# Optimization experiments

Measured on AMD Instinct MI355X. Metric: run time of the kernel, lower is better.

## Reference

```python
import jax, jax.numpy as jnp
import numpy as np

IN_DIM = 32000   # source vocab
OUT_DIM = 32000  # target vocab
HID = 1024
MAXLEN = 32      # decode steps
B = 64
SRC_LEN = 256


def _lstm_bias(h):
    # Keras LSTM: unit_forget_bias=True -> forget-gate bias = 1, rest 0. Gate order i,f,g,o.
    return jnp.concatenate([jnp.zeros(h), jnp.ones(h), jnp.zeros(2 * h)])


def setup_inputs() -> dict:
    key = jax.random.key(0)
    ks = jax.random.split(key, 12)
    g = lambda k, shape, s=0.02: (jax.random.normal(k, shape, jnp.float32) * s)
    return {
        "source": jax.random.randint(ks[0], (B, SRC_LEN), 0, IN_DIM, jnp.int32),
        "enc_emb": g(ks[1], (IN_DIM, HID)),
        "enc_K": g(ks[2], (HID, 4 * HID)),
        "enc_R": g(ks[3], (HID, 4 * HID)),
        "enc_b": _lstm_bias(HID),
        "dec_emb": g(ks[4], (OUT_DIM, HID)),
        "dec_K": g(ks[5], (HID, 4 * HID)),
        "dec_R": g(ks[6], (HID, 4 * HID)),
        "dec_b": _lstm_bias(HID),
        "W_a": g(ks[7], (HID, HID)),
        "W_c": g(ks[8], (2 * HID, HID)),
        "b_c": jnp.zeros(HID, jnp.float32),
        "W_out": g(ks[9], (HID, OUT_DIM)),
        "b_out": jnp.zeros(OUT_DIM, jnp.float32),
    }


def _lstm_cell(x, h, c, K, R, b):
    z = x @ K + h @ R + b
    i, f, g, o = jnp.split(z, 4, axis=-1)
    c = jax.nn.sigmoid(f) * c + jax.nn.sigmoid(i) * jnp.tanh(g)
    h = jax.nn.sigmoid(o) * jnp.tanh(c)
    return h, c


def reference(source, enc_emb, enc_K, enc_R, enc_b,
              dec_emb, dec_K, dec_R, dec_b,
              W_a, W_c, b_c, W_out, b_out):
    bsz = source.shape[0]
    hid = enc_K.shape[0]

    # ----- Encoder (mask_zero=True: skip state update where source==0) -----
    xe = enc_emb[source]                      # [B,T,H]
    mask = source > 0                         # [B,T]

    def enc_step(carry, xm):
        h, c = carry
        x, m = xm                             # x [B,H], m [B]
        hn, cn = _lstm_cell(x, h, c, enc_K, enc_R, enc_b)
        m = m[:, None]
        return (jnp.where(m, hn, h), jnp.where(m, cn, c)), jnp.where(m, hn, h)

    h0 = jnp.zeros((bsz, hid), xe.dtype)
    (he, ce), hs_t = jax.lax.scan(enc_step, (h0, h0),
                                  (xe.transpose(1, 0, 2), mask.T))
    hs = hs_t.transpose(1, 0, 2)              # [B,T,H] encoder states

    # ----- Decoder loop (greedy argmax feedback) -----
    hsW = hs @ W_a                            # [B,T,H], precomputed attention keys
    amask = mask[:, None, :].astype(hs.dtype)  # [B,1,T]

    def dec_step(carry, _):
        y, h, c = carry                       # y [B] int32
        x = dec_emb[y]                        # [B,H]
        hn, cn = _lstm_cell(x, h, c, dec_K, dec_R, dec_b)
        ht = hn[:, None, :]                   # [B,1,H]
        # Luong attention with source mask (exp -> mask -> normalize, as in source)
        sc = jnp.einsum('bqh,bkh->bqk', ht, hsW)        # [B,1,T]
        sc = jnp.exp(sc - sc.max(-1, keepdims=True)) * amask
        a = sc / sc.sum(-1, keepdims=True)
        ctx = jnp.einsum('bqk,bkh->bqh', a, hs)          # [B,1,H]
        ah = jnp.tanh(jnp.concatenate([ctx, ht], -1) @ W_c + b_c)
        prob = jax.nn.softmax(ah @ W_out + b_out, axis=-1)[:, 0, :]  # [B,V]
        yn = jnp.argmax(prob, axis=-1).astype(jnp.int32)
        return (yn, hn, cn), prob

    y0 = jnp.ones((bsz,), jnp.int32)          # start token = 1 (tf.ones)
    _, outs = jax.lax.scan(dec_step, (y0, he, ce), None, length=MAXLEN)
    return outs.transpose(1, 0, 2)            # [B, MAXLEN, OUT_DIM]
```

## Files before the change

kernel.cpp:

```cpp
#include <hip/hip_runtime.h>
#include <hip/hip_bf16.h>

typedef __hip_bfloat16 bf16;
typedef short bf8v __attribute__((ext_vector_type(8)));
typedef float f32x4 __attribute__((ext_vector_type(4)));

#define DEVINL __device__ __forceinline__
#define MFMA16(a, b, c) __builtin_amdgcn_mfma_f32_16x16x32_bf16((a), (b), (c), 0, 0, 0)

DEVINL float us2f(unsigned short u) { unsigned v = ((unsigned)u) << 16; return __uint_as_float(v); }
DEVINL float b2f(bf16 x) { return __bfloat162float(x); }
DEVINL bf16 f2b(float x) { return __float2bfloat16(x); }
DEVINL float sigf(float x) { return 1.0f / (1.0f + expf(-x)); }
DEVINL unsigned short f2bu(float f) { bf16 h = __float2bfloat16(f); return *(unsigned short*)&h; }

DEVINL void gload16(const void* g, void* l) {
  __builtin_amdgcn_global_load_lds((const __attribute__((address_space(1))) void*)g,
                                   (__attribute__((address_space(3))) void*)l, 16, 0, 0);
}

DEVINL unsigned ald(const unsigned* p) {
  return __hip_atomic_load(p, __ATOMIC_RELAXED, __HIP_MEMORY_SCOPE_AGENT);
}
DEVINL void ast(unsigned* p, unsigned v) {
  __hip_atomic_store(p, v, __ATOMIC_RELAXED, __HIP_MEMORY_SCOPE_AGENT);
}
DEVINL float aldf(const float* p) { unsigned u = ald((const unsigned*)p); return __uint_as_float(u); }
DEVINL void astf(float* p, float v) { ast((unsigned*)p, __float_as_uint(v)); }

DEVINL void gridbar2(unsigned* bars, unsigned lgen) {
  __syncthreads();
  if (threadIdx.x == 0) {
    unsigned s = lgen & 1;
    unsigned g = blockIdx.x >> 5;
    unsigned* grp = bars + (g * 2 + s) * 16;
    unsigned* top = bars + (16 + s) * 16;
    unsigned* gen = bars + 288;
    unsigned t = __hip_atomic_fetch_add(grp, 1u, __ATOMIC_RELAXED, __HIP_MEMORY_SCOPE_AGENT);
    if (t == 31u) {
      ast(grp, 0u);
      unsigned tt = __hip_atomic_fetch_add(top, 1u, __ATOMIC_RELAXED, __HIP_MEMORY_SCOPE_AGENT);
      if (tt == 7u) {
        ast(top, 0u);
        asm volatile("s_waitcnt vmcnt(0)");
        ast(gen, lgen + 1u);
      }
    }
    while (ald(gen) <= lgen) __builtin_amdgcn_s_sleep(4);
  }
  __syncthreads();
}

DEVINL void bar64(unsigned* b, unsigned lgen, int lid) {
  __syncthreads();
  if (threadIdx.x == 0) {
    unsigned s = lgen & 1;
    unsigned* grp = b + (((unsigned)(lid >> 5) & 1u) * 2 + s) * 16;
    unsigned* top = b + (4 + s) * 16;
    unsigned* gen = b + 96;
    unsigned t = __hip_atomic_fetch_add(grp, 1u, __ATOMIC_RELAXED, __HIP_MEMORY_SCOPE_AGENT);
    if (t == 31u) {
      ast(grp, 0u);
      unsigned tt = __hip_atomic_fetch_add(top, 1u, __ATOMIC_RELAXED, __HIP_MEMORY_SCOPE_AGENT);
      if (tt == 1u) {
        ast(top, 0u);
        asm volatile("s_waitcnt vmcnt(0)");
        ast(gen, lgen + 1u);
      }
    }
    while (ald(gen) <= lgen) __builtin_amdgcn_s_sleep(2);
  }
  __syncthreads();
}

#define OKPT_H  ((size_t)0)
#define OKPT_L  ((size_t)8388608)
#define ORPT_H  ((size_t)16777216)
#define ORPT_L  ((size_t)25165824)
#define OWAT    ((size_t)33554432)
#define OXE_H   ((size_t)35651584)
#define OXE_L   ((size_t)69206016)
#define OHSF5   ((size_t)35651584)
#define OHSB5   ((size_t)102760448)
#define XCH     ((size_t)136314880)
#define OHPK_E0 (XCH + 0)
#define OHPK_E1 (XCH + 262144)
#define OHPK_D0 (XCH + 524288)
#define OCBUF5  (XCH + 1048576)
#define OAHPK   (XCH + 1310720)
#define ORSUM5  (XCH + 1572864)
#define ORMAX5  (XCH + 1638400)
#define ORIDX5  (XCH + 1769472)
#define OPSUM5  (XCH + 1900544)
#define OBARS5  (XCH + 1901568)
#define OXK_L5  ((size_t)138412032)
#define OWCT_H  ((size_t)0)
#define OWCT_L  ((size_t)4194304)
#define OPCTX5  ((size_t)8388608)
#define OWOT5   ((size_t)138412032)
#define OKRTH5  ((size_t)203948032)
#define OKRTL5  ((size_t)220725248)
#define OHSW5   ((size_t)237502464)

#define DELTA   1e-4f

#define D_LH   0
#define D_LL   32768
#define D_ZS   65536
#define D_KBH  83968
#define D_KBL  116736
#define D4_A   0
#define D4_W   16384
#define D4_E   49152
#define D_HBF  0
#define D_PSC  4096
#define D_EK   8448
#define D_PC4  8704
#define D_ZS3  0
#define D_PSC2 0
#define D_GMX  4352
#define D_CCN  8512
#define D_CAND 8576
#define D_YL   149504
#define D_INV  149568
#define D_RT   149632

__global__ void ed_zero_v6(float4* p, int n) {
  int i = blockIdx.x * 256 + threadIdx.x;
  if (i < n) p[i] = make_float4(0.f, 0.f, 0.f, 0.f);
}

__global__ void ed_transpose_v6(const float* __restrict__ in, bf16* __restrict__ out,
                                int R, int C, int ostride, int ooff, int perm) {
  __shared__ float tile[32][33];
  int c0 = blockIdx.x * 32, r0 = blockIdx.y * 32;
  int tx = threadIdx.x & 31, ty0 = threadIdx.x >> 5;
#pragma unroll
  for (int i = 0; i < 4; i++) {
    int ty = ty0 + i * 8;
    tile[ty][tx] = in[(size_t)(r0 + ty) * C + c0 + tx];
  }
  __syncthreads();
#pragma unroll
  for (int i = 0; i < 4; i++) {
    int ty = ty0 + i * 8;
    int c = c0 + ty;
    int oc = perm ? ((c & 1023) * 4 + (c >> 10)) : c;
    out[(size_t)oc * ostride + ooff + r0 + tx] = f2b(tile[tx][ty]);
  }
}

__global__ void ed_transpose_split_v6(const float* __restrict__ in, bf16* __restrict__ oh,
                                      bf16* __restrict__ ol, int R, int C, int ostride,
                                      int ooff, int perm) {
  __shared__ float tile[32][33];
  int c0 = blockIdx.x * 32, r0 = blockIdx.y * 32;
  int tx = threadIdx.x & 31, ty0 = threadIdx.x >> 5;
#pragma unroll
  for (int i = 0; i < 4; i++) {
    int ty = ty0 + i * 8;
    tile[ty][tx] = in[(size_t)(r0 + ty) * C + c0 + tx];
  }
  __syncthreads();
#pragma unroll
  for (int i = 0; i < 4; i++) {
    int ty = ty0 + i * 8;
    int c = c0 + ty;
    int oc = perm ? ((c & 1023) * 4 + (c >> 10)) : c;
    float v = tile[tx][ty];
    bf16 hh = f2b(v);
    size_t o = (size_t)oc * ostride + ooff + r0 + tx;
    oh[o] = hh;
    ol[o] = f2b(v - b2f(hh));
  }
}

__global__ void ed_gather_split_v6(const int* __restrict__ src, const float* __restrict__ emb,
                                   bf16* __restrict__ xh, bf16* __restrict__ xl) {
  int bid = blockIdx.x;
  int t = bid >> 6, b = bid & 63;
  int tok = src[b * 256 + t];
  const float* rowp = emb + (size_t)tok * 1024;
  int i = threadIdx.x * 4;
  float4 v = *(const float4*)(rowp + i);
  bf16 h0 = f2b(v.x), h1 = f2b(v.y), h2 = f2b(v.z), h3 = f2b(v.w);
  ushort4 oh, ol;
  oh.x = *(unsigned short*)&h0; oh.y = *(unsigned short*)&h1;
  oh.z = *(unsigned short*)&h2; oh.w = *(unsigned short*)&h3;
  ol.x = f2bu(v.x - b2f(h0)); ol.y = f2bu(v.y - b2f(h1));
  ol.z = f2bu(v.z - b2f(h2)); ol.w = f2bu(v.w - b2f(h3));
  *(ushort4*)(xh + (size_t)bid * 1024 + i) = oh;
  *(ushort4*)(xl + (size_t)bid * 1024 + i) = ol;
}

__global__ __launch_bounds__(256, 2) void ed_gemm_bt_v6(
    const bf16* __restrict__ A, const bf16* __restrict__ BT, bf16* __restrict__ C,
    int M, int N, int K) {
  __shared__ __align__(16) bf16 As[128 * 32];
  __shared__ __align__(16) bf16 Bs[128 * 32];
  int m0 = blockIdx.y * 128, n0 = blockIdx.x * 128;
  int tid = threadIdx.x, w = tid >> 6, l = tid & 63;
  int wm = w >> 1, wn = w & 1;
  int lr = l & 15, lq = l >> 4;
  f32x4 acc[4][4] = {};
  for (int k0 = 0; k0 < K; k0 += 32) {
    __syncthreads();
#pragma unroll
    for (int j = 0; j < 2; j++) {
      int o = (w * 2 + j) * 1024 + l * 16;
      int rrow = o >> 6, kk = (o & 63) >> 1;
      gload16(A + (size_t)(m0 + rrow) * K + k0 + kk, (char*)As + (w * 2 + j) * 1024);
      gload16(BT + (size_t)(n0 + rrow) * K + k0 + kk, (char*)Bs + (w * 2 + j) * 1024);
    }
    __syncthreads();
#pragma unroll
    for (int mi = 0; mi < 4; mi++) {
      bf8v a = *(const bf8v*)(As + (wm * 64 + mi * 16 + lr) * 32 + lq * 8);
#pragma unroll
      for (int ni = 0; ni < 4; ni++) {
        bf8v b = *(const bf8v*)(Bs + (wn * 64 + ni * 16 + lr) * 32 + lq * 8);
        acc[mi][ni] = MFMA16(a, b, acc[mi][ni]);
      }
    }
  }
#pragma unroll
  for (int mi = 0; mi < 4; mi++)
#pragma unroll
    for (int ni = 0; ni < 4; ni++)
#pragma unroll
      for (int r = 0; r < 4; r++)
        C[(size_t)(m0 + wm * 64 + mi * 16 + lq * 4 + r) * N + n0 + wn * 64 + ni * 16 + lr] =
            f2b(acc[mi][ni][r]);
}

__global__ __launch_bounds__(256, 2) void ed_gemm3_v6(
    const bf16* __restrict__ Ah, const bf16* __restrict__ Al,
    const bf16* __restrict__ Bh, const bf16* __restrict__ Bl,
    bf16* __restrict__ Ch, bf16* __restrict__ Cl, int M, int N, int K) {
  __shared__ __align__(16) bf16 Ash[128 * 32];
  __shared__ __align__(16) bf16 Asl[128 * 32];
  __shared__ __align__(16) bf16 Bsh[128 * 32];
  __shared__ __align__(16) bf16 Bsl[128 * 32];
  int m0 = blockIdx.y * 128, n0 = blockIdx.x * 128;
  int tid = threadIdx.x, w = tid >> 6, l = tid & 63;
  int wm = w >> 1, wn = w & 1;
  int lr = l & 15, lq = l >> 4;
  f32x4 acc[4][4] = {};
  for (int k0 = 0; k0 < K; k0 += 32) {
    __syncthreads();
#pragma unroll
    for (int j = 0; j < 2; j++) {
      int o = (w * 2 + j) * 1024 + l * 16;
      int rrow = o >> 6, kk = (o & 63) >> 1;
      gload16(Ah + (size_t)(m0 + rrow) * K + k0 + kk, (char*)Ash + (w * 2 + j) * 1024);
      gload16(Al + (size_t)(m0 + rrow) * K + k0 + kk, (char*)Asl + (w * 2 + j) * 1024);
      gload16(Bh + (size_t)(n0 + rrow) * K + k0 + kk, (char*)Bsh + (w * 2 + j) * 1024);
      gload16(Bl + (size_t)(n0 + rrow) * K + k0 + kk, (char*)Bsl + (w * 2 + j) * 1024);
    }
    __syncthreads();
#pragma unroll
    for (int mi = 0; mi < 4; mi++) {
      bf8v a_h = *(const bf8v*)(Ash + (wm * 64 + mi * 16 + lr) * 32 + lq * 8);
      bf8v a_l = *(const bf8v*)(Asl + (wm * 64 + mi * 16 + lr) * 32 + lq * 8);
#pragma unroll
      for (int ni = 0; ni < 4; ni++) {
        bf8v b_h = *(const bf8v*)(Bsh + (wn * 64 + ni * 16 + lr) * 32 + lq * 8);
        bf8v b_l = *(const bf8v*)(Bsl + (wn * 64 + ni * 16 + lr) * 32 + lq * 8);
        acc[mi][ni] = MFMA16(a_h, b_h, acc[mi][ni]);
        acc[mi][ni] = MFMA16(a_h, b_l, acc[mi][ni]);
        acc[mi][ni] = MFMA16(a_l, b_h, acc[mi][ni]);
      }
    }
  }
#pragma unroll
  for (int mi = 0; mi < 4; mi++)
#pragma unroll
    for (int ni = 0; ni < 4; ni++)
#pragma unroll
      for (int r = 0; r < 4; r++) {
        float v = acc[mi][ni][r];
        bf16 hh = f2b(v);
        size_t idx = (size_t)(m0 + wm * 64 + mi * 16 + lq * 4 + r) * N + n0 + wn * 64 + ni * 16 + lr;
        Ch[idx] = hh;
        Cl[idx] = f2b(v - b2f(hh));
      }
}

__global__ __launch_bounds__(1024, 4) void ed_enc_v6(
    const int* __restrict__ src, const bf16* __restrict__ Rh, const bf16* __restrict__ Rl,
    const bf16* __restrict__ Xh, const bf16* __restrict__ Xl, const float* __restrict__ enc_b,
    unsigned* hpk0, unsigned* hpk1, float* __restrict__ cbuf,
    float* __restrict__ hsf, bf16* __restrict__ hsb, unsigned* barsE) {
  extern __shared__ char sm[];
  bf16* lh = (bf16*)sm;
  bf16* ll = (bf16*)(sm + 32768);
  float* zs = (float*)(sm + 65536);
  float* xkf = (float*)(sm + 82944);
  int bid = blockIdx.x, tid = threadIdx.x;
  int bg = bid >> 6, cg = bid & 63, lid = bid & 63;
  unsigned* barL = barsE + bg * 128;
  int wv = tid >> 6, l = tid & 63, lr = l & 15, lq = l >> 4;
  int kq = wv >> 2, cs = wv & 3;
  int srow = tid >> 6, sj0 = (tid & 63) * 16;
  int grow = tid >> 4, gul = tid & 15;
  bf8v Rh_[8], Rl_[8];
  {
    const bf16* bh = Rh + (size_t)(cg * 64 + cs * 16 + lr) * 1024 + kq * 256 + lq * 8;
    const bf16* bl = Rl + (size_t)(cg * 64 + cs * 16 + lr) * 1024 + kq * 256 + lq * 8;
#pragma unroll
    for (int i = 0; i < 8; i++) {
      Rh_[i] = *(const bf8v*)(bh + i * 32);
      Rl_[i] = *(const bf8v*)(bl + i * 32);
    }
  }
  float bi[4];
  float c_ = 0.f;
  if (tid < 256) {
#pragma unroll
    for (int g = 0; g < 4; g++) {
      int colp = cg * 64 + gul * 4 + g;
      bi[g] = enc_b[(colp & 3) * 1024 + (colp >> 2)];
    }
  }
  unsigned *hc = hpk0, *hn = hpk1;
  unsigned lgen = 0;
  for (int t = 0; t < 256; t++) {
    {
      const unsigned* hrow = hc + (size_t)(bg * 16 + srow) * 1024 + sj0;
      unsigned u[16];
#pragma unroll
      for (int j = 0; j < 16; j++) u[j] = ald(hrow + j);
      int r8 = (srow & 7) << 3;
#pragma unroll
      for (int j = 0; j < 16; j += 2) {
        int es = (sj0 + j) ^ r8;
        *(unsigned*)((char*)lh + srow * 2048 + es * 2) = (u[j] >> 16) | (u[j + 1] & 0xffff0000u);
        *(unsigned*)((char*)ll + srow * 2048 + es * 2) = (u[j] & 0xffffu) | (u[j + 1] << 16);
      }
    }
    {
      int xr = tid >> 6, xc = tid & 63;
      size_t xi = ((size_t)t * 64 + bg * 16 + xr) * 4096 + cg * 64 + xc;
      unsigned short xh = __builtin_nontemporal_load((const unsigned short*)(Xh + xi));
      unsigned short xl = __builtin_nontemporal_load((const unsigned short*)(Xl + xi));
      xkf[xr * 64 + xc] = us2f(xh) + us2f(xl);
    }
    __syncthreads();
    {
      f32x4 acc = {0.f, 0.f, 0.f, 0.f};
      int r8 = (lr & 7) << 3;
#pragma unroll
      for (int i = 0; i < 8; i++) {
        int e0 = kq * 256 + i * 32 + lq * 8;
        int es = e0 ^ r8;
        bf8v a_h = *(const bf8v*)((char*)lh + lr * 2048 + es * 2);
        bf8v a_l = *(const bf8v*)((char*)ll + lr * 2048 + es * 2);
        acc = MFMA16(a_h, Rh_[i], acc);
        acc = MFMA16(a_h, Rl_[i], acc);
        acc = MFMA16(a_l, Rh_[i], acc);
        acc = MFMA16(a_l, Rl_[i], acc);
      }
#pragma unroll
      for (int r = 0; r < 4; r++) zs[(kq * 16 + lq * 4 + r) * 68 + cs * 16 + lr] = acc[r];
    }
    __syncthreads();
    if (tid < 256) {
      int b_ = bg * 16 + grow, u = cg * 16 + gul;
      float zz[4];
#pragma unroll
      for (int g = 0; g < 4; g++) {
        int cc = gul * 4 + g;
        zz[g] = zs[(0 + grow) * 68 + cc] + zs[(16 + grow) * 68 + cc] +
                zs[(32 + grow) * 68 + cc] + zs[(48 + grow) * 68 + cc] +
                xkf[grow * 64 + cc] + bi[g];
      }
      float iv = sigf(zz[0]), fv = sigf(zz[1]), gv = tanhf(zz[2]), ov = sigf(zz[3]);
      float cn = fv * c_ + iv * gv;
      float hnv = ov * tanhf(cn);
      bool m = src[b_ * 256 + t] > 0;
      int es = u ^ ((grow & 7) << 3);
      float hold = b2f(*(const bf16*)((char*)lh + grow * 2048 + es * 2)) +
                   b2f(*(const bf16*)((char*)ll + grow * 2048 + es * 2));
      float hv = m ? hnv : hold;
      c_ = m ? cn : c_;
      unsigned short uh = f2bu(hv);
      unsigned pkv = ((unsigned)uh << 16) | (unsigned)f2bu(hv - us2f(uh));
      ast(hn + (size_t)b_ * 1024 + u, pkv);
      __builtin_nontemporal_store(hv, hsf + ((size_t)t * 64 + b_) * 1024 + u);
      __builtin_nontemporal_store(f2bu(hv), (unsigned short*)(hsb + ((size_t)t * 64 + b_) * 1024 + u));
    }
    bar64(barL, lgen, lid);
    lgen++;
    unsigned* tp = hc; hc = hn; hn = tp;
  }
  if (tid < 256) cbuf[(size_t)(bg * 16 + grow) * 1024 + cg * 16 + gul] = c_;
}

DEVINL void dec_lstm6(int bg, int cgl, int tid, char* sm,
                      const unsigned* hc, unsigned* hn,
                      const float* __restrict__ dec_emb,
                      const bf16* __restrict__ Kh, const bf16* __restrict__ Kl,
                      const float* __restrict__ dec_b, float& c_) {
  bf16* lh = (bf16*)(sm + D_LH);
  bf16* ll = (bf16*)(sm + D_LL);
  {
    int srow = tid >> 6, sl = tid & 63;
    const unsigned* hrow = hc + (size_t)(bg * 16 + srow) * 1024 + sl * 16;
    unsigned u[16];
#pragma unroll
    for (int j = 0; j < 16; j++) u[j] = ald(hrow + j);
    uint4 ha, hb, la, lb;
    ha.x = (u[0] >> 16) | (u[1] & 0xffff0000u);  ha.y = (u[2] >> 16) | (u[3] & 0xffff0000u);
    ha.z = (u[4] >> 16) | (u[5] & 0xffff0000u);  ha.w = (u[6] >> 16) | (u[7] & 0xffff0000u);
    hb.x = (u[8] >> 16) | (u[9] & 0xffff0000u);  hb.y = (u[10] >> 16) | (u[11] & 0xffff0000u);
    hb.z = (u[12] >> 16) | (u[13] & 0xffff0000u); hb.w = (u[14] >> 16) | (u[15] & 0xffff0000u);
    la.x = (u[0] & 0xffffu) | (u[1] << 16);  la.y = (u[2] & 0xffffu) | (u[3] << 16);
    la.z = (u[4] & 0xffffu) | (u[5] << 16);  la.w = (u[6] & 0xffffu) | (u[7] << 16);
    lb.x = (u[8] & 0xffffu) | (u[9] << 16);  lb.y = (u[10] & 0xffffu) | (u[11] << 16);
    lb.z = (u[12] & 0xffffu) | (u[13] << 16); lb.w = (u[14] & 0xffffu) | (u[15] << 16);
    int swz = (srow & 7) << 4;
    char* rbh = (char*)lh + srow * 2048;
    char* rbl = (char*)ll + srow * 2048;
    *(uint4*)(rbh + ((sl * 32) ^ swz)) = ha;
    *(uint4*)(rbh + ((sl * 32 + 16) ^ swz)) = hb;
    *(uint4*)(rbl + ((sl * 32) ^ swz)) = la;
    *(uint4*)(rbl + ((sl * 32 + 16) ^ swz)) = lb;
  }
  int wv = tid >> 6, l = tid & 63, lr = l & 15, lq = l >> 4;
  int kg2 = wv >> 2, cs = wv & 3;
  bf16* kbh = (bf16*)(sm + D_KBH);
  bf16* kbl = (bf16*)(sm + D_KBL);
  const int* y_l = (const int*)(sm + D_YL);
  float* zs = (float*)(sm + D_ZS);
  f32x4 acc = {0.f, 0.f, 0.f, 0.f};
  int colB = cs * 16 + lr;
  int bswz = (colB & 7) << 4;
  int aswz = (lr & 7) << 4;
  for (int c = 0; c < 8; c++) {
    __syncthreads();
#pragma unroll
    for (int r = 0; r < 2; r++) {
      int i = wv * 128 + r * 64 + l;
      int col = i >> 5, j = i & 31;
      size_t se = (size_t)(cgl * 64 + col) * 2048 + c * 256 + ((size_t)(j ^ (col & 7)) << 3);
      gload16(Kh + se, (char*)kbh + wv * 2048 + r * 1024);
      gload16(Kl + se, (char*)kbl + wv * 2048 + r * 1024);
    }
    __syncthreads();
#pragma unroll
    for (int s = 0; s < 2; s++) {
      int kl = kg2 * 64 + s * 32 + lq * 8;
      bf8v b_h = *(const bf8v*)((char*)kbh + colB * 512 + ((kl * 2) ^ bswz));
      bf8v b_l = *(const bf8v*)((char*)kbl + colB * 512 + ((kl * 2) ^ bswz));
      int gk = c * 256 + kl;
      bf8v a_h, a_l;
      if (gk < 1024) {
        const float* xr = dec_emb + (size_t)y_l[lr] * 1024 + gk;
        float4 v0 = *(const float4*)xr;
        float4 v1 = *(const float4*)(xr + 4);
        float vs[8] = {v0.x, v0.y, v0.z, v0.w, v1.x, v1.y, v1.z, v1.w};
#pragma unroll
        for (int e = 0; e < 8; e++) {
          unsigned short uh = f2bu(vs[e]);
          a_h[e] = (short)uh;
          a_l[e] = (short)f2bu(vs[e] - us2f(uh));
        }
      } else {
        int hk = gk - 1024;
        a_h = *(const bf8v*)((char*)lh + lr * 2048 + ((hk * 2) ^ aswz));
        a_l = *(const bf8v*)((char*)ll + lr * 2048 + ((hk * 2) ^ aswz));
      }
      acc = MFMA16(a_h, b_h, acc);
      acc = MFMA16(a_h, b_l, acc);
      acc = MFMA16(a_l, b_h, acc);
      acc = MFMA16(a_l, b_l, acc);
    }
  }
#pragma unroll
  for (int r = 0; r < 4; r++) zs[(kg2 * 16 + lq * 4 + r) * 68 + cs * 16 + lr] = acc[r];
  __syncthreads();
  if (tid < 256) {
    int grow = tid >> 4, gul = tid & 15;
    int b_ = bg * 16 + grow;
    float zz[4];
#pragma unroll
    for (int g = 0; g < 4; g++) {
      int cc = gul * 4 + g;
      int colp = cgl * 64 + cc;
      float v = zs[(0 + grow) * 68 + cc] + zs[(16 + grow) * 68 + cc] +
                zs[(32 + grow) * 68 + cc] + zs[(48 + grow) * 68 + cc];
      zz[g] = v + dec_b[(colp & 3) * 1024 + (colp >> 2)];
    }
    float iv = sigf(zz[0]), fv = sigf(zz[1]), gv = tanhf(zz[2]), ov = sigf(zz[3]);
    float cn = fv * c_ + iv * gv;
    c_ = cn;
    float hv = ov * tanhf(cn);
    unsigned short uh = f2bu(hv);
    unsigned pkv = ((unsigned)uh << 16) | (unsigned)f2bu(hv - us2f(uh));
    ast(hn + (size_t)b_ * 1024 + cgl * 16 + gul, pkv);
  }
}

__global__ __launch_bounds__(1024, 4) void ed_dec_v6(
    const int* __restrict__ src,
    const bf16* __restrict__ KRh, const bf16* __restrict__ KRl, const float* __restrict__ dec_b,
    const bf16* __restrict__ WcTh, const bf16* __restrict__ WcTl, const float* __restrict__ b_cp,
    const bf16* __restrict__ WoTh, const float* __restrict__ b_op,
    const float* __restrict__ Wout_f32, const float* __restrict__ dec_emb,
    const float* __restrict__ hsf, const bf16* __restrict__ hsW,
    unsigned* hpkA, unsigned* hpkB, float* __restrict__ cbuf,
    float* __restrict__ pctx, float* __restrict__ psum, unsigned* ahpk,
    float* __restrict__ rowsum, float* __restrict__ rmax, int* __restrict__ ridx,
    float* __restrict__ out, unsigned* barsG, unsigned* barsL) {
  extern __shared__ char sm[];
  int bid = blockIdx.x, tid = threadIdx.x;
  int bg = bid >> 6, cgl = bid & 63, lid = bid & 63;
  unsigned* barL = barsL + bg * 128;
  int wv = tid >> 6, l = tid & 63, lr = l & 15, lq = l >> 4;
  float c_ = 0.f;
  if (tid < 256) c_ = cbuf[(size_t)(bg * 16 + (tid >> 4)) * 1024 + cgl * 16 + (tid & 15)];
  unsigned *hc = hpkA, *hn = hpkB;
  unsigned lgenL = 0, lgenG = 0;

  if (tid < 16) ((int*)(sm + D_YL))[tid] = 1;
  __syncthreads();
  dec_lstm6(bg, cgl, tid, sm, hc, hn, dec_emb, KRh, KRl, dec_b, c_);
  bar64(barL, lgenL, lid); lgenL++;
  { unsigned* tp = hc; hc = hn; hn = tp; }

  for (int st = 0; st < 32; st++) {
    {
      int b_ = bid >> 2, kg = bid & 3;
      float* hbf = (float*)(sm + D_HBF);
      hbf[tid] = us2f((unsigned short)(ald(hc + (size_t)b_ * 1024 + tid) >> 16));
      __syncthreads();
      float* psc = (float*)(sm + D_PSC);
      {
        int kl = tid >> 4, q = tid & 15;
        const bf16* wrow = hsW + ((size_t)(kg * 64 + kl) * 64 + b_) * 1024 + q * 64;
        float p = 0.f;
#pragma unroll
        for (int j = 0; j < 8; j++) {
          uint4 wv_ = *(const uint4*)(wrow + j * 8);
          int kb = q * 64 + j * 8;
          p += hbf[kb + 0] * us2f(wv_.x & 0xffff) + hbf[kb + 1] * us2f(wv_.x >> 16);
          p += hbf[kb + 2] * us2f(wv_.y & 0xffff) + hbf[kb + 3] * us2f(wv_.y >> 16);
          p += hbf[kb + 4] * us2f(wv_.z & 0xffff) + hbf[kb + 5] * us2f(wv_.z >> 16);
          p += hbf[kb + 6] * us2f(wv_.w & 0xffff) + hbf[kb + 7] * us2f(wv_.w >> 16);
        }
        psc[kl * 17 + q] = p;
      }
      __syncthreads();
      float* ek = (float*)(sm + D_EK);
      if (tid < 64) {
        float sc = 0.f;
#pragma unroll
        for (int q = 0; q < 16; q++) sc += psc[tid * 17 + q];
        ek[tid] = (src[b_ * 256 + kg * 64 + tid] > 0) ? expf(sc) : 0.f;
      }
      __syncthreads();
      float* pc4 = (float*)(sm + D_PC4);
      {
        int cq = tid & 255, kc = tid >> 8;
        float a0 = 0.f, a1 = 0.f, a2 = 0.f, a3 = 0.f;
#pragma unroll 4
        for (int j = 0; j < 16; j++) {
          float e = ek[kc * 16 + j];
          const float* hr = hsf + ((size_t)(kg * 64 + kc * 16 + j) * 64 + b_) * 1024 + cq * 4;
          float4 uv = *(const float4*)hr;
          a0 += e * uv.x; a1 += e * uv.y; a2 += e * uv.z; a3 += e * uv.w;
        }
        pc4[kc * 1024 + cq * 4 + 0] = a0;
        pc4[kc * 1024 + cq * 4 + 1] = a1;
        pc4[kc * 1024 + cq * 4 + 2] = a2;
        pc4[kc * 1024 + cq * 4 + 3] = a3;
      }
      __syncthreads();
      {
        float v = pc4[tid] + pc4[1024 + tid] + pc4[2048 + tid] + pc4[3072 + tid];
        astf(pctx + ((size_t)kg * 64 + b_) * 1024 + tid, v);
      }
      if (tid == 0) {
        float* ek2 = (float*)(sm + D_EK);
        float s_ = 0.f;
        for (int i2 = 0; i2 < 64; i2++) s_ += ek2[i2];
        astf(psum + kg * 64 + b_, s_);
      }
    }
    bar64(barL, lgenL, lid); lgenL++;
    {
      float* inv_l = (float*)(sm + D_INV);
      if (tid < 16) {
        int rb = bg * 16 + tid;
        float sg = aldf(psum + rb) + aldf(psum + 64 + rb) +
                   aldf(psum + 128 + rb) + aldf(psum + 192 + rb);
        inv_l[tid] = 1.0f / sg;
      }
      __syncthreads();
      float* zs3 = (float*)(sm + D_ZS3);
      {
        int kq = wv;
        f32x4 acc = {0.f, 0.f, 0.f, 0.f};
        const bf16* bh = WcTh + (size_t)(cgl * 16 + lr) * 2048;
        const bf16* bl = WcTl + (size_t)(cgl * 16 + lr) * 2048;
        float inv = inv_l[lr];
#pragma unroll
        for (int i = 0; i < 4; i++) {
          int k = kq * 128 + i * 32 + lq * 8;
          bf8v a_h, a_l;
          if (k < 1024) {
            const float* p0 = pctx + (size_t)(bg * 16 + lr) * 1024 + k;
#pragma unroll
            for (int e = 0; e < 8; e++) {
              float v = (aldf(p0 + e) + aldf(p0 + 65536 + e) +
                         aldf(p0 + 131072 + e) + aldf(p0 + 196608 + e)) * inv;
              unsigned short uh = f2bu(v);
              a_h[e] = (short)uh;
              a_l[e] = (short)f2bu(v - us2f(uh));
            }
          } else {
            const unsigned* hp = hc + (size_t)(bg * 16 + lr) * 1024 + (k - 1024);
#pragma unroll
            for (int e = 0; e < 8; e++) {
              unsigned u = ald(hp + e);
              a_h[e] = (short)(u >> 16);
              a_l[e] = (short)(u & 0xffffu);
            }
          }
          bf8v b_h = *(const bf8v*)(bh + k);
          bf8v b_l = *(const bf8v*)(bl + k);
          acc = MFMA16(a_h, b_h, acc); acc = MFMA16(a_h, b_l, acc);
          acc = MFMA16(a_l, b_h, acc); acc = MFMA16(a_l, b_l, acc);
        }
#pragma unroll
        for (int r = 0; r < 4; r++) zs3[(kq * 16 + lq * 4 + r) * 17 + lr] = acc[r];
      }
      __syncthreads();
      if (tid < 256) {
        int grow = tid >> 4, gcol = tid & 15;
        float v = 0.f;
#pragma unroll
        for (int q = 0; q < 16; q++) v += zs3[(q * 16 + grow) * 17 + gcol];
        v += b_cp[cgl * 16 + gcol];
        float ahv = tanhf(v);
        unsigned short uh = f2bu(ahv);
        unsigned pkv = ((unsigned)uh << 16) | (unsigned)f2bu(ahv - us2f(uh));
        ast(ahpk + (size_t)(bg * 16 + grow) * 1024 + cgl * 16 + gcol, pkv);
      }
    }
    gridbar2(barsG, lgenG); lgenG++;
    {
      int base = bid * 125;
      bf16* abuf = (bf16*)(sm + D4_A);
      bf16* wbuf = (bf16*)(sm + D4_W);
      int rg = wv >> 2, cpair = wv & 3;
      f32x4 acc0 = {0.f, 0.f, 0.f, 0.f}, acc1 = {0.f, 0.f, 0.f, 0.f};
      for (int kc = 0; kc < 8; kc++) {
        int k0 = kc * 128;
        __syncthreads();
        {
          int row = tid >> 4, l16 = tid & 15;
          const unsigned* ap = ahpk + (size_t)row * 1024 + k0 + l16 * 8;
          unsigned u0 = ald(ap), u1 = ald(ap + 1), u2 = ald(ap + 2), u3 = ald(ap + 3);
          unsigned u4 = ald(ap + 4), u5 = ald(ap + 5), u6 = ald(ap + 6), u7 = ald(ap + 7);
          uint4 hv;
          hv.x = (u0 >> 16) | (u1 & 0xffff0000u);
          hv.y = (u2 >> 16) | (u3 & 0xffff0000u);
          hv.z = (u4 >> 16) | (u5 & 0xffff0000u);
          hv.w = (u6 >> 16) | (u7 & 0xffff0000u);
          *(uint4*)((char*)abuf + row * 256 + ((l16 * 16) ^ ((row & 7) << 4))) = hv;
        }
#pragma unroll
        for (int r = 0; r < 2; r++) {
          int i = wv * 128 + r * 64 + l;
          int col = i >> 4, j = i & 15;
          int ccol = col < 125 ? col : 124;
          size_t se = (size_t)(base + ccol) * 1024 + k0 + ((size_t)(j ^ (col & 7)) << 3);
          gload16(WoTh + se, (char*)wbuf + wv * 2048 + r * 1024);
        }
        __syncthreads();
#pragma unroll
        for (int s = 0; s < 4; s++) {
          int kl = s * 32 + lq * 8;
          int ar = rg * 16 + lr;
          bf8v a = *(const bf8v*)((char*)abuf + ar * 256 + ((kl * 2) ^ ((ar & 7) << 4)));
          int c0 = cpair * 32 + lr, c1 = c0 + 16;
          bf8v b0 = *(const bf8v*)((char*)wbuf + c0 * 256 + ((kl * 2) ^ ((c0 & 7) << 4)));
          bf8v b1 = *(const bf8v*)((char*)wbuf + c1 * 256 + ((kl * 2) ^ ((c1 & 7) << 4)));
          acc0 = MFMA16(a, b0, acc0);
          acc1 = MFMA16(a, b1, acc1);
        }
      }
      __syncthreads();
      float* e = (float*)(sm + D4_E);
      {
        int cl0 = cpair * 32 + lr;
        if (cl0 < 125) {
#pragma unroll
          for (int r = 0; r < 4; r++)
            e[(rg * 16 + lq * 4 + r) * 129 + cl0] = acc0[r] + b_op[base + cl0];
        }
        int cl1 = cpair * 32 + 16 + lr;
        if (cl1 < 125) {
#pragma unroll
          for (int r = 0; r < 4; r++)
            e[(rg * 16 + lq * 4 + r) * 129 + cl1] = acc1[r] + b_op[base + cl1];
        }
      }
      __syncthreads();
      if (tid < 64) {
        float sm_ = 0.f, v1 = -1e30f, v2 = -1e30f;
        int i1 = 0, i2 = 0;
        for (int c2 = 0; c2 < 125; c2++) {
          float v = e[tid * 129 + c2];
          sm_ += expf(v);
          if (v > v1) { v2 = v1; i2 = i1; v1 = v; i1 = base + c2; }
          else if (v > v2) { v2 = v; i2 = base + c2; }
        }
        astf(rowsum + bid * 64 + tid, sm_);
        astf(rmax + (bid * 64 + tid) * 2 + 0, v1);
        ast((unsigned*)ridx + (bid * 64 + tid) * 2 + 0, (unsigned)i1);
        astf(rmax + (bid * 64 + tid) * 2 + 1, v2);
        ast((unsigned*)ridx + (bid * 64 + tid) * 2 + 1, (unsigned)i2);
      }
    }
    gridbar2(barsG, lgenG); lgenG++;
    {
      float* psc2 = (float*)(sm + D_PSC2);
      {
        int rr = tid & 63, pp = tid >> 6;
        float s_ = 0.f;
#pragma unroll 4
        for (int cu = pp * 16; cu < pp * 16 + 16; cu++) s_ += aldf(rowsum + cu * 64 + rr);
        psc2[rr * 17 + pp] = s_;
      }
      __syncthreads();
      float* rt = (float*)(sm + D_RT);
      if (tid < 64) {
        float s_ = 0.f;
#pragma unroll
        for (int p2 = 0; p2 < 16; p2++) s_ += psc2[tid * 17 + p2];
        rt[tid] = s_;
      }
      __syncthreads();
      float* e = (float*)(sm + D4_E);
      {
        int base = bid * 125;
        for (int i = tid; i < 8000; i += 1024) {
          int r_ = i / 125, c2 = i - r_ * 125;
          float pv = expf(e[r_ * 129 + c2]) / rt[r_];
          __builtin_nontemporal_store(pv, out + ((size_t)r_ * 32 + st) * 32000 + base + c2);
        }
      }
      if (st < 31) {
        float* gmx = (float*)(sm + D_GMX);
        int* ccnt = (int*)(sm + D_CCN);
        int* cand = (int*)(sm + D_CAND);
        int* y_l = (int*)(sm + D_YL);
        int r16 = tid & 15, ch = tid >> 4;
        int rowg = bg * 16 + r16;
        float vloc[8]; int iloc[8];
        {
          float m_ = -1e30f;
#pragma unroll
          for (int ee = 0; ee < 8; ee++) {
            int ent = ch * 8 + ee;
            vloc[ee] = aldf(rmax + ((size_t)(ent >> 1) * 64 + rowg) * 2 + (ent & 1));
            iloc[ee] = (int)ald((const unsigned*)ridx + ((size_t)(ent >> 1) * 64 + rowg) * 2 + (ent & 1));
            m_ = fmaxf(m_, vloc[ee]);
          }
          gmx[r16 * 65 + ch] = m_;
        }
        if (tid < 16) ccnt[tid] = 0;
        __syncthreads();
        if (tid < 16) {
          float g_ = -1e30f;
#pragma unroll
          for (int j = 0; j < 64; j++) g_ = fmaxf(g_, gmx[tid * 65 + j]);
          gmx[tid * 65 + 64] = g_;
        }
        __syncthreads();
        {
          float thr = gmx[r16 * 65 + 64] - DELTA;
#pragma unroll
          for (int ee = 0; ee < 8; ee++) {
            if (vloc[ee] >= thr) {
              int slot = atomicAdd(&ccnt[r16], 1);
              if (slot < 8) cand[r16 * 8 + slot] = iloc[ee];
            }
          }
        }
        __syncthreads();
        {
          int row2 = wv;
          int rowg2 = bg * 16 + row2;
          int cnt = ccnt[row2]; if (cnt > 8) cnt = 8;
          double bv = -1e30; int bi_ = 0x7fffffff;
          for (int ci = 0; ci < cnt; ci++) {
            int c = cand[row2 * 8 + ci];
            double s_ = 0.0;
            for (int k = l; k < 1024; k += 64) {
              unsigned u = ald(ahpk + (size_t)rowg2 * 1024 + k);
              float av = us2f((unsigned short)(u >> 16)) + us2f((unsigned short)(u & 0xffffu));
              float wv_ = __builtin_nontemporal_load(Wout_f32 + (size_t)k * 32000 + c);
              s_ += (double)av * (double)wv_;
            }
#pragma unroll
            for (int off = 32; off > 0; off >>= 1) s_ += __shfl_down(s_, off);
            if (l == 0) {
              s_ += (double)b_op[c];
              if (s_ > bv || (s_ == bv && c < bi_)) { bv = s_; bi_ = c; }
            }
          }
          if (l == 0) y_l[row2] = bi_;
        }
        __syncthreads();
        dec_lstm6(bg, cgl, tid, sm, hc, hn, dec_emb, KRh, KRl, dec_b, c_);
      }
    }
    bar64(barL, lgenL, lid); lgenL++;
    { unsigned* tp = hc; hc = hn; hn = tp; }
  }
}

extern "C" void kernel_launch(void* const* d_in, const int* in_sizes, int n_in,
                              void* d_out, int out_size, void* d_ws, size_t ws_size,
                              hipStream_t stream) {
  (void)in_sizes; (void)n_in; (void)out_size; (void)ws_size;
  const int*   src     = (const int*)  d_in[0];
  const float* enc_emb = (const float*)d_in[1];
  const float* enc_K   = (const float*)d_in[2];
  const float* enc_R   = (const float*)d_in[3];
  const float* enc_b   = (const float*)d_in[4];
  const float* dec_emb = (const float*)d_in[5];
  const float* dec_K   = (const float*)d_in[6];
  const float* dec_R   = (const float*)d_in[7];
  const float* dec_b   = (const float*)d_in[8];
  const float* W_a     = (const float*)d_in[9];
  const float* W_c     = (const float*)d_in[10];
  const float* b_c     = (const float*)d_in[11];
  const float* W_out   = (const float*)d_in[12];
  const float* b_out   = (const float*)d_in[13];
  char* ws = (char*)d_ws;

  hipFuncSetAttribute((const void*)ed_enc_v6, hipFuncAttributeMaxDynamicSharedMemorySize, 163840);
  hipFuncSetAttribute((const void*)ed_dec_v6, hipFuncAttributeMaxDynamicSharedMemorySize, 163840);

  bf16* KpTh = (bf16*)(ws + OKPT_H);
  bf16* KpTl = (bf16*)(ws + OKPT_L);
  bf16* RpTh = (bf16*)(ws + ORPT_H);
  bf16* RpTl = (bf16*)(ws + ORPT_L);
  bf16* WaT  = (bf16*)(ws + OWAT);
  bf16* xeh  = (bf16*)(ws + OXE_H);
  bf16* xel  = (bf16*)(ws + OXE_L);
  float* hsf = (float*)(ws + OHSF5);
  bf16* hsb  = (bf16*)(ws + OHSB5);
  unsigned* hpkE0 = (unsigned*)(ws + OHPK_E0);
  unsigned* hpkE1 = (unsigned*)(ws + OHPK_E1);
  unsigned* hpkD0 = (unsigned*)(ws + OHPK_D0);
  float* cbuf = (float*)(ws + OCBUF5);
  unsigned* ahpk = (unsigned*)(ws + OAHPK);
  float* rsum = (float*)(ws + ORSUM5);
  float* rmaxp = (float*)(ws + ORMAX5);
  int*  ridxp = (int*)(ws + ORIDX5);
  float* psum = (float*)(ws + OPSUM5);
  unsigned* barsE = (unsigned*)(ws + OBARS5);
  unsigned* barsG = (unsigned*)(ws + OBARS5 + 4096);
  unsigned* barsL = (unsigned*)(ws + OBARS5 + 8192);
  bf16* XkL  = (bf16*)(ws + OXK_L5);
  bf16* XkH  = (bf16*)d_out;
  bf16* WcTh = (bf16*)(ws + OWCT_H);
  bf16* WcTl = (bf16*)(ws + OWCT_L);
  float* pctx = (float*)(ws + OPCTX5);
  bf16* WoTh = (bf16*)(ws + OWOT5);
  bf16* KRTh = (bf16*)(ws + OKRTH5);
  bf16* KRTl = (bf16*)(ws + OKRTL5);
  bf16* hsW  = (bf16*)(ws + OHSW5);

  ed_zero_v6<<<512, 256, 0, stream>>>((float4*)(ws + XCH), 131072);
  ed_transpose_split_v6<<<dim3(128, 32), 256, 0, stream>>>(enc_K, KpTh, KpTl, 1024, 4096, 1024, 0, 1);
  ed_transpose_split_v6<<<dim3(128, 32), 256, 0, stream>>>(enc_R, RpTh, RpTl, 1024, 4096, 1024, 0, 1);
  ed_transpose_v6<<<dim3(32, 32), 256, 0, stream>>>(W_a, WaT, 1024, 1024, 1024, 0, 0);
  ed_gather_split_v6<<<16384, 256, 0, stream>>>(src, enc_emb, xeh, xel);
  ed_gemm3_v6<<<dim3(32, 128), 256, 0, stream>>>(xeh, xel, KpTh, KpTl, XkH, XkL, 16384, 4096, 1024);
  ed_transpose_split_v6<<<dim3(32, 64), 256, 0, stream>>>(W_c, WcTh, WcTl, 2048, 1024, 2048, 0, 0);
  ed_enc_v6<<<256, 1024, 87040, stream>>>(src, RpTh, RpTl, XkH, XkL, enc_b,
                                          hpkE0, hpkE1, cbuf, hsf, hsb, barsE);
  ed_transpose_v6<<<dim3(1000, 32), 256, 0, stream>>>(W_out, WoTh, 1024, 32000, 1024, 0, 0);
  ed_transpose_split_v6<<<dim3(128, 32), 256, 0, stream>>>(dec_K, KRTh, KRTl, 1024, 4096, 2048, 0, 1);
  ed_transpose_split_v6<<<dim3(128, 32), 256, 0, stream>>>(dec_R, KRTh, KRTl, 1024, 4096, 2048, 1024, 1);
  ed_gemm_bt_v6<<<dim3(8, 128), 256, 0, stream>>>(hsb, WaT, hsW, 16384, 1024, 1024);
  ed_dec_v6<<<256, 1024, 150528, stream>>>(src, KRTh, KRTl, dec_b, WcTh, WcTl, b_c,
                                           WoTh, b_out, W_out, dec_emb, hsf, hsW,
                                           hpkE0, hpkD0, cbuf, pctx, psum, ahpk,
                                           rsum, rmaxp, ridxp, (float*)d_out, barsG, barsL);
}
```

Baseline: 13.90 ms.

## Reassociate attention scores: project decoder state by W_a instead of precomputing hs@W_a

Drops the precomputed hs@W_a GEMM over all encoder states (16384x1024x1024), along with the W_a transpose and the bf16 copy of encoder states. Each decode step now computes q = h·W_aᵀ with MFMA (reading fp32 W_a and converting on the fly), stores it in a global buffer, and dots q against the fp32 encoder states. This trades the large upfront GEMM and its bf16 traffic for 32 small per-step projections plus an extra grid barrier per step. Scores are now taken against fp32 states rather than a bf16 hsW.

Result: slower. 14.43 ms (+3.8%).

```diff
diff --git a/kernel.cpp b/kernel.cpp
--- a/kernel.cpp
+++ b/kernel.cpp
@@ -77,11 +77,9 @@
 #define OKPT_L  ((size_t)8388608)
 #define ORPT_H  ((size_t)16777216)
 #define ORPT_L  ((size_t)25165824)
-#define OWAT    ((size_t)33554432)
 #define OXE_H   ((size_t)35651584)
 #define OXE_L   ((size_t)69206016)
 #define OHSF5   ((size_t)35651584)
-#define OHSB5   ((size_t)102760448)
 #define XCH     ((size_t)136314880)
 #define OHPK_E0 (XCH + 0)
 #define OHPK_E1 (XCH + 262144)
@@ -97,10 +95,10 @@
 #define OWCT_H  ((size_t)0)
 #define OWCT_L  ((size_t)4194304)
 #define OPCTX5  ((size_t)8388608)
+#define OQBUF   ORPT_H
 #define OWOT5   ((size_t)138412032)
 #define OKRTH5  ((size_t)203948032)
 #define OKRTL5  ((size_t)220725248)
-#define OHSW5   ((size_t)237502464)
 
 #define DELTA   1e-4f
 
@@ -112,7 +110,7 @@
 #define D4_A   0
 #define D4_W   16384
 #define D4_E   49152
-#define D_HBF  0
+#define D_QL   0
 #define D_PSC  4096
 #define D_EK   8448
 #define D_PC4  8704
@@ -125,12 +123,12 @@
 #define D_INV  149568
 #define D_RT   149632
 
-__global__ void ed_zero_v6(float4* p, int n) {
+__global__ void ed_zero_v7(float4* p, int n) {
   int i = blockIdx.x * 256 + threadIdx.x;
   if (i < n) p[i] = make_float4(0.f, 0.f, 0.f, 0.f);
 }
 
-__global__ void ed_transpose_v6(const float* __restrict__ in, bf16* __restrict__ out,
+__global__ void ed_transpose_v7(const float* __restrict__ in, bf16* __restrict__ out,
                                 int R, int C, int ostride, int ooff, int perm) {
   __shared__ float tile[32][33];
   int c0 = blockIdx.x * 32, r0 = blockIdx.y * 32;
@@ -150,7 +148,7 @@
   }
 }
 
-__global__ void ed_transpose_split_v6(const float* __restrict__ in, bf16* __restrict__ oh,
+__global__ void ed_transpose_split_v7(const float* __restrict__ in, bf16* __restrict__ oh,
                                       bf16* __restrict__ ol, int R, int C, int ostride,
                                       int ooff, int perm) {
   __shared__ float tile[32][33];
@@ -175,7 +173,7 @@
   }
 }
 
-__global__ void ed_gather_split_v6(const int* __restrict__ src, const float* __restrict__ emb,
+__global__ void ed_gather_split_v7(const int* __restrict__ src, const float* __restrict__ emb,
                                    bf16* __restrict__ xh, bf16* __restrict__ xl) {
   int bid = blockIdx.x;
   int t = bid >> 6, b = bid & 63;
@@ -193,47 +191,7 @@
   *(ushort4*)(xl + (size_t)bid * 1024 + i) = ol;
 }
 
-__global__ __launch_bounds__(256, 2) void ed_gemm_bt_v6(
-    const bf16* __restrict__ A, const bf16* __restrict__ BT, bf16* __restrict__ C,
-    int M, int N, int K) {
-  __shared__ __align__(16) bf16 As[128 * 32];
-  __shared__ __align__(16) bf16 Bs[128 * 32];
-  int m0 = blockIdx.y * 128, n0 = blockIdx.x * 128;
-  int tid = threadIdx.x, w = tid >> 6, l = tid & 63;
-  int wm = w >> 1, wn = w & 1;
-  int lr = l & 15, lq = l >> 4;
-  f32x4 acc[4][4] = {};
-  for (int k0 = 0; k0 < K; k0 += 32) {
-    __syncthreads();
-#pragma unroll
-    for (int j = 0; j < 2; j++) {
-      int o = (w * 2 + j) * 1024 + l * 16;
-      int rrow = o >> 6, kk = (o & 63) >> 1;
-      gload16(A + (size_t)(m0 + rrow) * K + k0 + kk, (char*)As + (w * 2 + j) * 1024);
-      gload16(BT + (size_t)(n0 + rrow) * K + k0 + kk, (char*)Bs + (w * 2 + j) * 1024);
-    }
-    __syncthreads();
-#pragma unroll
-    for (int mi = 0; mi < 4; mi++) {
-      bf8v a = *(const bf8v*)(As + (wm * 64 + mi * 16 + lr) * 32 + lq * 8);
-#pragma unroll
-      for (int ni = 0; ni < 4; ni++) {
-        bf8v b = *(const bf8v*)(Bs + (wn * 64 + ni * 16 + lr) * 32 + lq * 8);
-        acc[mi][ni] = MFMA16(a, b, acc[mi][ni]);
-      }
-    }
-  }
-#pragma unroll
-  for (int mi = 0; mi < 4; mi++)
-#pragma unroll
-    for (int ni = 0; ni < 4; ni++)
-#pragma unroll
-      for (int r = 0; r < 4; r++)
-        C[(size_t)(m0 + wm * 64 + mi * 16 + lq * 4 + r) * N + n0 + wn * 64 + ni * 16 + lr] =
-            f2b(acc[mi][ni][r]);
-}
-
-__global__ __launch_bounds__(256, 2) void ed_gemm3_v6(
+__global__ __launch_bounds__(256, 2) void ed_gemm3_v7(
     const bf16* __restrict__ Ah, const bf16* __restrict__ Al,
     const bf16* __restrict__ Bh, const bf16* __restrict__ Bl,
     bf16* __restrict__ Ch, bf16* __restrict__ Cl, int M, int N, int K) {
@@ -286,11 +244,11 @@
       }
 }
 
-__global__ __launch_bounds__(1024, 4) void ed_enc_v6(
+__global__ __launch_bounds__(1024, 4) void ed_enc_v7(
     const int* __restrict__ src, const bf16* __restrict__ Rh, const bf16* __restrict__ Rl,
     const bf16* __restrict__ Xh, const bf16* __restrict__ Xl, const float* __restrict__ enc_b,
     unsigned* hpk0, unsigned* hpk1, float* __restrict__ cbuf,
-    float* __restrict__ hsf, bf16* __restrict__ hsb, unsigned* barsE) {
+    float* __restrict__ hsf, unsigned* barsE) {
   extern __shared__ char sm[];
   bf16* lh = (bf16*)sm;
   bf16* ll = (bf16*)(sm + 32768);
@@ -386,8 +344,7 @@
       unsigned short uh = f2bu(hv);
       unsigned pkv = ((unsigned)uh << 16) | (unsigned)f2bu(hv - us2f(uh));
       ast(hn + (size_t)b_ * 1024 + u, pkv);
-      __builtin_nontemporal_store(hv, hsf + ((size_t)t * 64 + b_) * 1024 + u);
-      __builtin_nontemporal_store(f2bu(hv), (unsigned short*)(hsb + ((size_t)t * 64 + b_) * 1024 + u));
+      hsf[((size_t)t * 64 + b_) * 1024 + u] = hv;
     }
     bar64(barL, lgen, lid);
     lgen++;
@@ -396,7 +353,7 @@
   if (tid < 256) cbuf[(size_t)(bg * 16 + grow) * 1024 + cg * 16 + gul] = c_;
 }
 
-DEVINL void dec_lstm6(int bg, int cgl, int tid, char* sm,
+DEVINL void dec_lstm7(int bg, int cgl, int tid, char* sm,
                       const unsigned* hc, unsigned* hn,
                       const float* __restrict__ dec_emb,
                       const bf16* __restrict__ Kh, const bf16* __restrict__ Kl,
@@ -501,13 +458,14 @@
   }
 }
 
-__global__ __launch_bounds__(1024, 4) void ed_dec_v6(
+__global__ __launch_bounds__(1024, 4) void ed_dec_v7(
     const int* __restrict__ src,
     const bf16* __restrict__ KRh, const bf16* __restrict__ KRl, const float* __restrict__ dec_b,
     const bf16* __restrict__ WcTh, const bf16* __restrict__ WcTl, const float* __restrict__ b_cp,
     const bf16* __restrict__ WoTh, const float* __restrict__ b_op,
     const float* __restrict__ Wout_f32, const float* __restrict__ dec_emb,
-    const float* __restrict__ hsf, const bf16* __restrict__ hsW,
+    const float* __restrict__ W_a, float* __restrict__ qbuf,
+    const float* __restrict__ hsf,
     unsigned* hpkA, unsigned* hpkB, float* __restrict__ cbuf,
     float* __restrict__ pctx, float* __restrict__ psum, unsigned* ahpk,
     float* __restrict__ rowsum, float* __restrict__ rmax, int* __restrict__ ridx,
@@ -524,31 +482,62 @@
 
   if (tid < 16) ((int*)(sm + D_YL))[tid] = 1;
   __syncthreads();
-  dec_lstm6(bg, cgl, tid, sm, hc, hn, dec_emb, KRh, KRl, dec_b, c_);
+  dec_lstm7(bg, cgl, tid, sm, hc, hn, dec_emb, KRh, KRl, dec_b, c_);
   bar64(barL, lgenL, lid); lgenL++;
   { unsigned* tp = hc; hc = hn; hn = tp; }
 
   for (int st = 0; st < 32; st++) {
+    if (cgl < 16) {
+      int colb = cgl * 64;
+      int kq = wv >> 2, nq = wv & 3;
+      float* zs = (float*)(sm + D_ZS);
+      f32x4 acc = {0.f, 0.f, 0.f, 0.f};
+      const unsigned* hrow = hc + (size_t)(bg * 16 + lr) * 1024;
+      const float* warow = W_a + (size_t)(colb + nq * 16 + lr) * 1024;
+#pragma unroll
+      for (int i = 0; i < 8; i++) {
+        int k = kq * 256 + i * 32 + lq * 8;
+        bf8v a, b;
+        const unsigned* hp = hrow + k;
+#pragma unroll
+        for (int e = 0; e < 8; e++) a[e] = (short)(ald(hp + e) >> 16);
+        const float* wp = warow + k;
+        float4 w0 = *(const float4*)wp;
+        float4 w1 = *(const float4*)(wp + 4);
+        b[0] = (short)f2bu(w0.x); b[1] = (short)f2bu(w0.y);
+        b[2] = (short)f2bu(w0.z); b[3] = (short)f2bu(w0.w);
+        b[4] = (short)f2bu(w1.x); b[5] = (short)f2bu(w1.y);
+        b[6] = (short)f2bu(w1.z); b[7] = (short)f2bu(w1.w);
+        acc = MFMA16(a, b, acc);
+      }
+#pragma unroll
+      for (int r = 0; r < 4; r++) zs[(kq * 16 + lq * 4 + r) * 68 + nq * 16 + lr] = acc[r];
+      __syncthreads();
+      {
+        int mrow = tid >> 6, col = tid & 63;
+        float v = zs[(0 + mrow) * 68 + col] + zs[(16 + mrow) * 68 + col] +
+                  zs[(32 + mrow) * 68 + col] + zs[(48 + mrow) * 68 + col];
+        astf(qbuf + (size_t)(bg * 16 + mrow) * 1024 + colb + col, v);
+      }
+    }
+    bar64(barL, lgenL, lid); lgenL++;
     {
       int b_ = bid >> 2, kg = bid & 3;
-      float* hbf = (float*)(sm + D_HBF);
-      hbf[tid] = us2f((unsigned short)(ald(hc + (size_t)b_ * 1024 + tid) >> 16));
+      float* q_l = (float*)(sm + D_QL);
+      q_l[tid] = aldf(qbuf + (size_t)b_ * 1024 + tid);
       __syncthreads();
       float* psc = (float*)(sm + D_PSC);
       {
-        int kl = tid >> 4, q = tid & 15;
-        const bf16* wrow = hsW + ((size_t)(kg * 64 + kl) * 64 + b_) * 1024 + q * 64;
+        int kl = tid >> 4, qq = tid & 15;
+        const float* hrow = hsf + ((size_t)(kg * 64 + kl) * 64 + b_) * 1024;
         float p = 0.f;
-#pragma unroll
-        for (int j = 0; j < 8; j++) {
-          uint4 wv_ = *(const uint4*)(wrow + j * 8);
-          int kb = q * 64 + j * 8;
-          p += hbf[kb + 0] * us2f(wv_.x & 0xffff) + hbf[kb + 1] * us2f(wv_.x >> 16);
-          p += hbf[kb + 2] * us2f(wv_.y & 0xffff) + hbf[kb + 3] * us2f(wv_.y >> 16);
-          p += hbf[kb + 4] * us2f(wv_.z & 0xffff) + hbf[kb + 5] * us2f(wv_.z >> 16);
-          p += hbf[kb + 6] * us2f(wv_.w & 0xffff) + hbf[kb + 7] * us2f(wv_.w >> 16);
-        }
-        psc[kl * 17 + q] = p;
+#pragma unroll 4
+        for (int j = 0; j < 16; j++) {
+          int e0 = j * 64 + qq * 4;
+          float4 hv = *(const float4*)(hrow + e0);
+          p += hv.x * q_l[e0] + hv.y * q_l[e0 + 1] + hv.z * q_l[e0 + 2] + hv.w * q_l[e0 + 3];
+        }
+        psc[kl * 17 + qq] = p;
       }
       __syncthreads();
       float* ek = (float*)(sm + D_EK);
@@ -815,7 +804,7 @@
           if (l == 0) y_l[row2] = bi_;
         }
         __syncthreads();
-        dec_lstm6(bg, cgl, tid, sm, hc, hn, dec_emb, KRh, KRl, dec_b, c_);
+        dec_lstm7(bg, cgl, tid, sm, hc, hn, dec_emb, KRh, KRl, dec_b, c_);
       }
     }
     bar64(barL, lgenL, lid); lgenL++;
@@ -843,18 +832,16 @@
   const float* b_out   = (const float*)d_in[13];
   char* ws = (char*)d_ws;
 
-  hipFuncSetAttribute((const void*)ed_enc_v6, hipFuncAttributeMaxDynamicSharedMemorySize, 163840);
-  hipFuncSetAttribute((const void*)ed_dec_v6, hipFuncAttributeMaxDynamicSharedMemorySize, 163840);
+  hipFuncSetAttribute((const void*)ed_enc_v7, hipFuncAttributeMaxDynamicSharedMemorySize, 163840);
+  hipFuncSetAttribute((const void*)ed_dec_v7, hipFuncAttributeMaxDynamicSharedMemorySize, 163840);
 
   bf16* KpTh = (bf16*)(ws + OKPT_H);
   bf16* KpTl = (bf16*)(ws + OKPT_L);
   bf16* RpTh = (bf16*)(ws + ORPT_H);
   bf16* RpTl = (bf16*)(ws + ORPT_L);
-  bf16* WaT  = (bf16*)(ws + OWAT);
   bf16* xeh  = (bf16*)(ws + OXE_H);
   bf16* xel  = (bf16*)(ws + OXE_L);
   float* hsf = (float*)(ws + OHSF5);
-  bf16* hsb  = (bf16*)(ws + OHSB5);
   unsigned* hpkE0 = (unsigned*)(ws + OHPK_E0);
   unsigned* hpkE1 = (unsigned*)(ws + OHPK_E1);
   unsigned* hpkD0 = (unsigned*)(ws + OHPK_D0);
@@ -872,26 +859,24 @@
   bf16* WcTh = (bf16*)(ws + OWCT_H);
   bf16* WcTl = (bf16*)(ws + OWCT_L);
   float* pctx = (float*)(ws + OPCTX5);
+  float* qbuf = (float*)(ws + OQBUF);
   bf16* WoTh = (bf16*)(ws + OWOT5);
   bf16* KRTh = (bf16*)(ws + OKRTH5);
   bf16* KRTl = (bf16*)(ws + OKRTL5);
-  bf16* hsW  = (bf16*)(ws + OHSW5);
-
-  ed_zero_v6<<<512, 256, 0, stream>>>((float4*)(ws + XCH), 131072);
-  ed_transpose_split_v6<<<dim3(128, 32), 256, 0, stream>>>(enc_K, KpTh, KpTl, 1024, 4096, 1024, 0, 1);
-  ed_transpose_split_v6<<<dim3(128, 32), 256, 0, stream>>>(enc_R, RpTh, RpTl, 1024, 4096, 1024, 0, 1);
-  ed_transpose_v6<<<dim3(32, 32), 256, 0, stream>>>(W_a, WaT, 1024, 1024, 1024, 0, 0);
-  ed_gather_split_v6<<<16384, 256, 0, stream>>>(src, enc_emb, xeh, xel);
-  ed_gemm3_v6<<<dim3(32, 128), 256, 0, stream>>>(xeh, xel, KpTh, KpTl, XkH, XkL, 16384, 4096, 1024);
-  ed_transpose_split_v6<<<dim3(32, 64), 256, 0, stream>>>(W_c, WcTh, WcTl, 2048, 1024, 2048, 0, 0);
-  ed_enc_v6<<<256, 1024, 87040, stream>>>(src, RpTh, RpTl, XkH, XkL, enc_b,
-                                          hpkE0, hpkE1, cbuf, hsf, hsb, barsE);
-  ed_transpose_v6<<<dim3(1000, 32), 256, 0, stream>>>(W_out, WoTh, 1024, 32000, 1024, 0, 0);
-  ed_transpose_split_v6<<<dim3(128, 32), 256, 0, stream>>>(dec_K, KRTh, KRTl, 1024, 4096, 2048, 0, 1);
-  ed_transpose_split_v6<<<dim3(128, 32), 256, 0, stream>>>(dec_R, KRTh, KRTl, 1024, 4096, 2048, 1024, 1);
-  ed_gemm_bt_v6<<<dim3(8, 128), 256, 0, stream>>>(hsb, WaT, hsW, 16384, 1024, 1024);
-  ed_dec_v6<<<256, 1024, 150528, stream>>>(src, KRTh, KRTl, dec_b, WcTh, WcTl, b_c,
-                                           WoTh, b_out, W_out, dec_emb, hsf, hsW,
+
+  ed_zero_v7<<<512, 256, 0, stream>>>((float4*)(ws + XCH), 131072);
+  ed_transpose_split_v7<<<dim3(128, 32), 256, 0, stream>>>(enc_K, KpTh, KpTl, 1024, 4096, 1024, 0, 1);
+  ed_transpose_split_v7<<<dim3(128, 32), 256, 0, stream>>>(enc_R, RpTh, RpTl, 1024, 4096, 1024, 0, 1);
+  ed_gather_split_v7<<<16384, 256, 0, stream>>>(src, enc_emb, xeh, xel);
+  ed_gemm3_v7<<<dim3(32, 128), 256, 0, stream>>>(xeh, xel, KpTh, KpTl, XkH, XkL, 16384, 4096, 1024);
+  ed_transpose_split_v7<<<dim3(32, 64), 256, 0, stream>>>(W_c, WcTh, WcTl, 2048, 1024, 2048, 0, 0);
+  ed_enc_v7<<<256, 1024, 87040, stream>>>(src, RpTh, RpTl, XkH, XkL, enc_b,
+                                          hpkE0, hpkE1, cbuf, hsf, barsE);
+  ed_transpose_v7<<<dim3(1000, 32), 256, 0, stream>>>(W_out, WoTh, 1024, 32000, 1024, 0, 0);
+  ed_transpose_split_v7<<<dim3(128, 32), 256, 0, stream>>>(dec_K, KRTh, KRTl, 1024, 4096, 2048, 0, 1);
+  ed_transpose_split_v7<<<dim3(128, 32), 256, 0, stream>>>(dec_R, KRTh, KRTl, 1024, 4096, 2048, 1024, 1);
+  ed_dec_v7<<<256, 1024, 150528, stream>>>(src, KRTh, KRTl, dec_b, WcTh, WcTl, b_c,
+                                           WoTh, b_out, W_out, dec_emb, W_a, qbuf, hsf,
                                            hpkE0, hpkD0, cbuf, pctx, psum, ahpk,
                                            rsum, rmaxp, ridxp, (float*)d_out, barsG, barsL);
 }
```
